# Kernel optimization log

Measured on AMD Instinct MI355X. Metric: run time of the kernel, lower is better.

The kernel has to match this reference:

```python
import jax, jax.numpy as jnp
import numpy as np

N = 11616          # IMDB total nodes (hard-coded slices in source)
NHID = 512
L = 4              # num_layers (encoder and decoder each)
E = 371712         # ~32 avg degree
SIZES = [4278, 2081, 5257]
FEATS = [3066, 2081, 5257]
GAMMA = 3.0


def setup_inputs() -> dict:
    key = jax.random.key(0)
    ks = jax.random.split(key, 24)
    s = 0.02
    d = {}
    d["X0"] = jax.random.normal(ks[0], (SIZES[0], FEATS[0]), jnp.float32)
    d["X1"] = jax.random.normal(ks[1], (SIZES[1], FEATS[1]), jnp.float32)
    d["X2"] = jax.random.normal(ks[2], (SIZES[2], FEATS[2]), jnp.float32)
    d["src"] = jax.random.randint(ks[3], (E,), 0, N)
    d["dst"] = jax.random.randint(ks[4], (E,), 0, N)
    d["edge_w"] = jax.random.uniform(ks[5], (E,), jnp.float32) / 32.0  # ~normalized adjacency values
    d["adj_full"] = (jax.random.uniform(ks[6], (N, N), jnp.float32) < 0.005).astype(jnp.float32)
    # input projections fc_list: feat_dim -> nhid
    for i in range(3):
        d[f"fc_W{i}"] = jax.random.normal(ks[7 + i], (FEATS[i], NHID), jnp.float32) * s
        d[f"fc_b{i}"] = jnp.zeros((NHID,), jnp.float32)
    # stacked GraphConvolution weights (encoder / decoder)
    d["enc_W"] = jax.random.normal(ks[10], (L, NHID, NHID), jnp.float32) * s
    d["enc_b"] = jnp.zeros((L, NHID), jnp.float32)
    d["dec_W"] = jax.random.normal(ks[11], (L, NHID, NHID), jnp.float32) * s
    d["dec_b"] = jnp.zeros((L, NHID), jnp.float32)
    # output projections fc_list2: nhid -> feat_dim
    for i in range(3):
        d[f"out_W{i}"] = jax.random.normal(ks[12 + i], (NHID, FEATS[i]), jnp.float32) * s
        d[f"out_b{i}"] = jnp.zeros((FEATS[i],), jnp.float32)
    return d


def reference(X0, X1, X2, edge_w, adj_full,
              fc_W0, fc_b0, fc_W1, fc_b1, fc_W2, fc_b2,
              enc_W, enc_b, dec_W, dec_b,
              out_W0, out_b0, out_W1, out_b1, out_W2, out_b2,
              src, dst):
    def spmm(h):  # sparse A @ h via edge list
        return jax.ops.segment_sum(h[src] * edge_w[:, None], dst, num_segments=N)

    # per-type input projection, concat over node types -> [N, NHID]
    x = jnp.concatenate([X0 @ fc_W0 + fc_b0,
                         X1 @ fc_W1 + fc_b1,
                         X2 @ fc_W2 + fc_b2], axis=0)

    # encoder then decoder; per source: relu+dropout only at layer 0 (L>1 branch),
    # residual add for layers i>0; dropout is identity in eval mode.
    for W, b in ((enc_W, enc_b), (dec_W, dec_b)):
        for i in range(L):
            h = spmm(x @ W[i]) + b[i]
            x = jax.nn.relu(h) if i == 0 else x + h

    # IMDB slices of final embedding
    e0, e1, e2 = x[:SIZES[0]], x[SIZES[0]:SIZES[0] + SIZES[1]], x[SIZES[0] + SIZES[1]:]
    r0 = e0 @ out_W0 + out_b0
    r1 = e1 @ out_W1 + out_b1
    r2 = e2 @ out_W2 + out_b2

    # emb_loss_fun2: BCE(sigmoid(x x^T), adj_full), mean. Stable form:
    z = x @ x.T  # [N, N]
    emb_loss = jnp.mean(adj_full * jax.nn.softplus(-z) + (1.0 - adj_full) * jax.nn.softplus(z))

    # recon_loss_fun2 on type-0 features (cosine-based, power gamma)
    rn = r0 / jnp.maximum(jnp.linalg.norm(r0, axis=-1, keepdims=True), 1e-12)
    fn = X0 / jnp.maximum(jnp.linalg.norm(X0, axis=1, keepdims=True), 1e-12)
    recon_loss = jnp.mean((1.0 - jnp.sum(rn * fn, axis=-1)) ** GAMMA)

    return (r0, r1, r2, emb_loss, recon_loss)
```

## Files before the change

### kernel.cpp

```cpp
#include <hip/hip_runtime.h>
#include <math.h>

#define N_NODES 11616
#define NROWPAD 11776
#define NHID    512
#define EDGES   371712
#define S0 4278
#define S1 2081
#define S2 5257
#define F0 3066
#define F1 2081
#define F2 5257
#define NBLK 91
#define FC_KS 4

typedef __attribute__((ext_vector_type(8))) short bf16x8;
typedef __attribute__((ext_vector_type(4))) float f32x4;

#define GL2LDS(g, l) __builtin_amdgcn_global_load_lds(                         \
    (const __attribute__((address_space(1))) unsigned int*)(g),                \
    (__attribute__((address_space(3))) unsigned int*)(l), 16, 0, 0)

__device__ __forceinline__ int slot_of(int row, int kg)
{
    return row * 4 + (kg ^ ((row >> 1) & 3));
}

__global__ void k_init(double* __restrict__ accum, int* __restrict__ indeg,
                       int* __restrict__ cursor)
{
    int i = blockIdx.x * blockDim.x + threadIdx.x;
    if (i < 2) accum[i] = 0.0;
    if (i < N_NODES) { indeg[i] = 0; cursor[i] = 0; }
}

__global__ void k_padzero(short* __restrict__ xh, short* __restrict__ xl)
{
    int i = blockIdx.x * blockDim.x + threadIdx.x;
    const int base  = N_NODES * NHID;
    const int total = (NROWPAD - N_NODES) * NHID;
    if (i < total) { xh[base + i] = 0; xl[base + i] = 0; }
}

__global__ void k_count(const int* __restrict__ dst, int* __restrict__ indeg)
{
    int e = blockIdx.x * blockDim.x + threadIdx.x;
    if (e < EDGES) atomicAdd(&indeg[dst[e]], 1);
}

__global__ void k_scan(const int* __restrict__ indeg, int* __restrict__ rowptr)
{
    __shared__ int part[256];
    const int t = threadIdx.x;
    const int chunk = (N_NODES + 255) / 256;
    const int base = t * chunk;
    int s = 0;
    for (int i = 0; i < chunk; ++i) {
        int idx = base + i;
        if (idx < N_NODES) s += indeg[idx];
    }
    part[t] = s;
    __syncthreads();
    if (t == 0) for (int i = 1; i < 256; ++i) part[i] += part[i - 1];
    __syncthreads();
    int run = (t == 0) ? 0 : part[t - 1];
    for (int i = 0; i < chunk; ++i) {
        int idx = base + i;
        if (idx < N_NODES) { rowptr[idx] = run; run += indeg[idx]; }
    }
    if (t == 0) rowptr[N_NODES] = part[255];
}

__global__ void k_fill(const int* __restrict__ src, const int* __restrict__ dst,
                       const float* __restrict__ ew, const int* __restrict__ rowptr,
                       int* __restrict__ cursor, int* __restrict__ csrc,
                       float* __restrict__ cw)
{
    int e = blockIdx.x * blockDim.x + threadIdx.x;
    if (e >= EDGES) return;
    int d = dst[e];
    int pos = rowptr[d] + atomicAdd(&cursor[d], 1);
    csrc[pos] = src[e];
    cw[pos]   = ew[e];
}

__device__ __forceinline__ void split_bf16(float f, short& hi, short& lo)
{
    unsigned u  = __float_as_uint(f);
    unsigned hr = (u + 0x7FFFu + ((u >> 16) & 1u)) & 0xFFFF0000u;
    float    fh = __uint_as_float(hr);
    float    fl = f - fh;
    unsigned ul = __float_as_uint(fl);
    unsigned lr = ul + 0x7FFFu + ((ul >> 16) & 1u);
    hi = (short)(hr >> 16);
    lo = (short)(lr >> 16);
}

__global__ void k_splitpad(const float* __restrict__ in, short* __restrict__ oh,
                           short* __restrict__ ol, int R, int C, int Cpad)
{
    const int c = blockIdx.x * 256 + threadIdx.x;
    const int r = blockIdx.y;
    if (c >= Cpad) return;
    float f = (r < R && c < C) ? in[(long)r * C + c] : 0.f;
    short h, l;
    split_bf16(f, h, l);
    oh[(long)r * Cpad + c] = h;
    ol[(long)r * Cpad + c] = l;
}

__global__ void k_tsplit(const float* __restrict__ in, short* __restrict__ oh,
                         short* __restrict__ ol, int R, int C, int Rpad, int Cpad)
{
    __shared__ float tile[32][33];
    const int cb = blockIdx.x * 32, rb = blockIdx.y * 32;
    const int tx = threadIdx.x, ty = threadIdx.y;
    #pragma unroll
    for (int i = ty; i < 32; i += 8) {
        int r = rb + i, c = cb + tx;
        tile[i][tx] = (r < R && c < C) ? in[(long)r * C + c] : 0.f;
    }
    __syncthreads();
    #pragma unroll
    for (int i = ty; i < 32; i += 8) {
        int row = cb + i, col = rb + tx;
        if (row < Cpad && col < Rpad) {
            short h, l;
            split_bf16(tile[tx][i], h, l);
            oh[(long)row * Rpad + col] = h;
            ol[(long)row * Rpad + col] = l;
        }
    }
}

__device__ __forceinline__ void stage_gl(const short* __restrict__ src, int ldk,
                                         int k0, short* ldsPanel, int lane)
{
    #pragma unroll
    for (int i = 0; i < 8; ++i) {
        int ci  = i * 64 + lane;
        int row = ci >> 2;
        int kgs = (ci & 3) ^ ((row >> 1) & 3);
        const short* g = src + (long)row * ldk + k0 + kgs * 8;
        GL2LDS(g, (char*)ldsPanel + i * 1024);
    }
}

__global__ __launch_bounds__(256, 3)
void k_gemm_bb(const short* __restrict__ Agh, const short* __restrict__ Agl,
               const short* __restrict__ Bgh, const short* __restrict__ Bgl,
               const float* __restrict__ bias, float* __restrict__ C,
               int M, int NN, int Kpad, int ldk)
{
    __shared__ short P[4][4096];
    const int t = threadIdx.x, lane = t & 63, w = t >> 6;
    const int rowBase = blockIdx.y * 128, colBase = blockIdx.x * 128;
    const int wm = (w >> 1) * 64, wn = (w & 1) * 64;
    const int kg = lane >> 4, fr = lane & 15;

    const short* srcs[4] = { Agh + (long)rowBase * ldk, Agl + (long)rowBase * ldk,
                             Bgh + (long)colBase * ldk, Bgl + (long)colBase * ldk };
    const short* mySrc = srcs[w];

    int offA[4], offB[4];
    #pragma unroll
    for (int f = 0; f < 4; ++f) {
        int rA = wm + f * 16 + fr, rB = wn + f * 16 + fr;
        offA[f] = slot_of(rA, kg) * 8;
        offB[f] = slot_of(rB, kg) * 8;
    }

    f32x4 acc[4][4];
    #pragma unroll
    for (int i = 0; i < 4; ++i)
        #pragma unroll
        for (int j = 0; j < 4; ++j)
            acc[i][j] = (f32x4){0.f, 0.f, 0.f, 0.f};

    for (int k0 = 0; k0 < Kpad; k0 += 32) {
        stage_gl(mySrc, ldk, k0, &P[w][0], lane);
        __syncthreads();
        bf16x8 ah[4], al[4], bh[4], bl[4];
        #pragma unroll
        for (int f = 0; f < 4; ++f) {
            ah[f] = *(const bf16x8*)&P[0][offA[f]];
            al[f] = *(const bf16x8*)&P[1][offA[f]];
            bh[f] = *(const bf16x8*)&P[2][offB[f]];
            bl[f] = *(const bf16x8*)&P[3][offB[f]];
        }
        #pragma unroll
        for (int i = 0; i < 4; ++i)
            #pragma unroll
            for (int j = 0; j < 4; ++j) {
                acc[i][j] = __builtin_amdgcn_mfma_f32_16x16x32_bf16(ah[i], bh[j], acc[i][j], 0, 0, 0);
                acc[i][j] = __builtin_amdgcn_mfma_f32_16x16x32_bf16(ah[i], bl[j], acc[i][j], 0, 0, 0);
                acc[i][j] = __builtin_amdgcn_mfma_f32_16x16x32_bf16(al[i], bh[j], acc[i][j], 0, 0, 0);
            }
        __syncthreads();
    }

    #pragma unroll
    for (int i = 0; i < 4; ++i) {
        #pragma unroll
        for (int q = 0; q < 4; ++q) {
            int r = rowBase + wm + i * 16 + kg * 4 + q;
            if (r >= M) continue;
            #pragma unroll
            for (int j = 0; j < 4; ++j) {
                int c = colBase + wn + j * 16 + fr;
                if (c < NN)
                    C[(long)r * NN + c] = acc[i][j][q] + (bias ? bias[c] : 0.f);
            }
        }
    }
}

__global__ __launch_bounds__(256, 3)
void k_gemm_red(const short* __restrict__ Agh, const short* __restrict__ Agl,
                const short* __restrict__ Bgh, const short* __restrict__ Bgl,
                float* __restrict__ Cpart, int M, int ldk, int kChunk)
{
    __shared__ short P[4][4096];
    const int t = threadIdx.x, lane = t & 63, w = t >> 6;
    const int rowBase = blockIdx.y * 128, colBase = blockIdx.x * 128;
    const int z = blockIdx.z;
    const int wm = (w >> 1) * 64, wn = (w & 1) * 64;
    const int kg = lane >> 4, fr = lane & 15;

    const short* srcs[4] = { Agh + (long)rowBase * ldk, Agl + (long)rowBase * ldk,
                             Bgh + (long)colBase * ldk, Bgl + (long)colBase * ldk };
    const short* mySrc = srcs[w];

    int offA[4], offB[4];
    #pragma unroll
    for (int f = 0; f < 4; ++f) {
        int rA = wm + f * 16 + fr, rB = wn + f * 16 + fr;
        offA[f] = slot_of(rA, kg) * 8;
        offB[f] = slot_of(rB, kg) * 8;
    }

    f32x4 acc[4][4];
    #pragma unroll
    for (int i = 0; i < 4; ++i)
        #pragma unroll
        for (int j = 0; j < 4; ++j)
            acc[i][j] = (f32x4){0.f, 0.f, 0.f, 0.f};

    const int kEnd = z * kChunk + kChunk;
    for (int k0 = z * kChunk; k0 < kEnd; k0 += 32) {
        stage_gl(mySrc, ldk, k0, &P[w][0], lane);
        __syncthreads();
        bf16x8 ah[4], al[4], bh[4], bl[4];
        #pragma unroll
        for (int f = 0; f < 4; ++f) {
            ah[f] = *(const bf16x8*)&P[0][offA[f]];
            al[f] = *(const bf16x8*)&P[1][offA[f]];
            bh[f] = *(const bf16x8*)&P[2][offB[f]];
            bl[f] = *(const bf16x8*)&P[3][offB[f]];
        }
        #pragma unroll
        for (int i = 0; i < 4; ++i)
            #pragma unroll
            for (int j = 0; j < 4; ++j) {
                acc[i][j] = __builtin_amdgcn_mfma_f32_16x16x32_bf16(ah[i], bh[j], acc[i][j], 0, 0, 0);
                acc[i][j] = __builtin_amdgcn_mfma_f32_16x16x32_bf16(ah[i], bl[j], acc[i][j], 0, 0, 0);
                acc[i][j] = __builtin_amdgcn_mfma_f32_16x16x32_bf16(al[i], bh[j], acc[i][j], 0, 0, 0);
            }
        __syncthreads();
    }

    #pragma unroll
    for (int i = 0; i < 4; ++i) {
        #pragma unroll
        for (int q = 0; q < 4; ++q) {
            int r = rowBase + wm + i * 16 + kg * 4 + q;
            if (r >= M) continue;
            #pragma unroll
            for (int j = 0; j < 4; ++j) {
                int c = colBase + wn + j * 16 + fr;
                Cpart[((long)z * M + r) * NHID + c] = acc[i][j][q];
            }
        }
    }
}

__global__ void k_fcreduce(const float* __restrict__ Cpart, const float* __restrict__ bias,
                           int M, float* __restrict__ xo, short* __restrict__ oh,
                           short* __restrict__ ol)
{
    const int r = blockIdx.x;
    const int c = threadIdx.x << 2;
    float4 s = *reinterpret_cast<const float4*>(bias + c);
    #pragma unroll
    for (int z = 0; z < FC_KS; ++z) {
        const float4 p = *reinterpret_cast<const float4*>(Cpart + ((long)z * M + r) * NHID + c);
        s.x += p.x; s.y += p.y; s.z += p.z; s.w += p.w;
    }
    *reinterpret_cast<float4*>(xo + (long)r * NHID + c) = s;
    short4 h, l;
    split_bf16(s.x, h.x, l.x); split_bf16(s.y, h.y, l.y);
    split_bf16(s.z, h.z, l.z); split_bf16(s.w, h.w, l.w);
    *reinterpret_cast<short4*>(oh + (long)r * NHID + c) = h;
    *reinterpret_cast<short4*>(ol + (long)r * NHID + c) = l;
}

__global__ __launch_bounds__(256, 3)
void k_zloss(const short* __restrict__ xh, const short* __restrict__ xl,
             const float* __restrict__ adj, double* __restrict__ accum)
{
    __shared__ short P[4][4096];
    __shared__ float ztr[4][16][17];
    __shared__ float red[256];
    const int t = threadIdx.x, lane = t & 63, w = t >> 6;

    int b = blockIdx.x, R = 0;
    while (b >= NBLK - R) { b -= NBLK - R; ++R; }
    const int Cb = R + b;
    const int rowBase = R * 128, colBase = Cb * 128;
    const int diag = (Cb == R);

    const int wm = (w >> 1) * 64, wn = (w & 1) * 64;
    const int kg = lane >> 4, fr = lane & 15;

    const short* srcs[4] = { xh + (long)rowBase * NHID, xl + (long)rowBase * NHID,
                             xh + (long)colBase * NHID, xl + (long)colBase * NHID };
    const short* mySrc = srcs[w];

    int offA[4], offB[4];
    #pragma unroll
    for (int f = 0; f < 4; ++f) {
        int rA = wm + f * 16 + fr, rB = wn + f * 16 + fr;
        offA[f] = slot_of(rA, kg) * 8;
        offB[f] = slot_of(rB, kg) * 8;
    }

    f32x4 acc[4][4];
    #pragma unroll
    for (int i = 0; i < 4; ++i)
        #pragma unroll
        for (int j = 0; j < 4; ++j)
            acc[i][j] = (f32x4){0.f, 0.f, 0.f, 0.f};

    for (int k0 = 0; k0 < NHID; k0 += 32) {
        stage_gl(mySrc, NHID, k0, &P[w][0], lane);
        __syncthreads();
        bf16x8 ah[4], al[4], bh[4], bl[4];
        #pragma unroll
        for (int f = 0; f < 4; ++f) {
            ah[f] = *(const bf16x8*)&P[0][offA[f]];
            al[f] = *(const bf16x8*)&P[1][offA[f]];
            bh[f] = *(const bf16x8*)&P[2][offB[f]];
            bl[f] = *(const bf16x8*)&P[3][offB[f]];
        }
        #pragma unroll
        for (int i = 0; i < 4; ++i)
            #pragma unroll
            for (int j = 0; j < 4; ++j) {
                acc[i][j] = __builtin_amdgcn_mfma_f32_16x16x32_bf16(ah[i], bh[j], acc[i][j], 0, 0, 0);
                acc[i][j] = __builtin_amdgcn_mfma_f32_16x16x32_bf16(ah[i], bl[j], acc[i][j], 0, 0, 0);
                acc[i][j] = __builtin_amdgcn_mfma_f32_16x16x32_bf16(al[i], bh[j], acc[i][j], 0, 0, 0);
            }
        __syncthreads();
    }

    float local = 0.f;
    #pragma unroll
    for (int i = 0; i < 4; ++i) {
        #pragma unroll
        for (int q = 0; q < 4; ++q) {
            int r = rowBase + wm + i * 16 + kg * 4 + q;
            if (r >= N_NODES) continue;
            #pragma unroll
            for (int j = 0; j < 4; ++j) {
                int c = colBase + wn + j * 16 + fr;
                if (c >= N_NODES) continue;
                float z  = acc[i][j][q];
                float e  = __expf(-fabsf(z));
                float sp = fmaxf(z, 0.f) + __logf(1.f + e);
                float a1 = adj[(long)r * N_NODES + c];
                local += diag ? (sp - a1 * z) : (2.f * sp - a1 * z);
            }
        }
    }
    if (!diag) {
        #pragma unroll
        for (int i = 0; i < 4; ++i) {
            #pragma unroll
            for (int j = 0; j < 4; ++j) {
                #pragma unroll
                for (int q = 0; q < 4; ++q)
                    ztr[w][kg * 4 + q][fr] = acc[i][j][q];
                #pragma unroll
                for (int q = 0; q < 4; ++q) {
                    float zt = ztr[w][fr][kg * 4 + q];
                    int cc = colBase + wn + j * 16 + kg * 4 + q;
                    int rr = rowBase + wm + i * 16 + fr;
                    if (cc < N_NODES && rr < N_NODES)
                        local -= adj[(long)cc * N_NODES + rr] * zt;
                }
            }
        }
    }
    red[t] = local;
    __syncthreads();
    for (int sft = 128; sft > 0; sft >>= 1) {
        if (t < sft) red[t] += red[t + sft];
        __syncthreads();
    }
    if (t == 0) atomicAdd(accum, (double)red[0]);
}

__global__ void k_spmm(const float* __restrict__ y, const float* __restrict__ xold,
                       const int* __restrict__ rowptr, const int* __restrict__ csrc,
                       const float* __restrict__ cw, const float* __restrict__ bias,
                       int do_relu, float* __restrict__ xnew,
                       short* __restrict__ xh, short* __restrict__ xl)
{
    const int wv   = threadIdx.x >> 6;
    const int lane = threadIdx.x & 63;
    const int n    = blockIdx.x * 4 + wv;
    const int c1   = lane << 2;
    const int c2   = c1 + 256;
    float4 s1 = make_float4(0.f, 0.f, 0.f, 0.f);
    float4 s2 = make_float4(0.f, 0.f, 0.f, 0.f);
    const int beg = rowptr[n], end = rowptr[n + 1];
    for (int e = beg; e < end; ++e) {
        int   sn = csrc[e];
        float wt = cw[e];
        const float* yr = y + (long)sn * NHID;
        const float4 y1 = *reinterpret_cast<const float4*>(yr + c1);
        const float4 y2 = *reinterpret_cast<const float4*>(yr + c2);
        s1.x = fmaf(wt, y1.x, s1.x); s1.y = fmaf(wt, y1.y, s1.y);
        s1.z = fmaf(wt, y1.z, s1.z); s1.w = fmaf(wt, y1.w, s1.w);
        s2.x = fmaf(wt, y2.x, s2.x); s2.y = fmaf(wt, y2.y, s2.y);
        s2.z = fmaf(wt, y2.z, s2.z); s2.w = fmaf(wt, y2.w, s2.w);
    }
    const float4 b1 = *reinterpret_cast<const float4*>(bias + c1);
    const float4 b2 = *reinterpret_cast<const float4*>(bias + c2);
    float4 o1, o2;
    o1.x = s1.x + b1.x; o1.y = s1.y + b1.y; o1.z = s1.z + b1.z; o1.w = s1.w + b1.w;
    o2.x = s2.x + b2.x; o2.y = s2.y + b2.y; o2.z = s2.z + b2.z; o2.w = s2.w + b2.w;
    if (do_relu) {
        o1.x = fmaxf(o1.x, 0.f); o1.y = fmaxf(o1.y, 0.f);
        o1.z = fmaxf(o1.z, 0.f); o1.w = fmaxf(o1.w, 0.f);
        o2.x = fmaxf(o2.x, 0.f); o2.y = fmaxf(o2.y, 0.f);
        o2.z = fmaxf(o2.z, 0.f); o2.w = fmaxf(o2.w, 0.f);
    } else {
        const float4 x1 = *reinterpret_cast<const float4*>(xold + (long)n * NHID + c1);
        const float4 x2 = *reinterpret_cast<const float4*>(xold + (long)n * NHID + c2);
        o1.x += x1.x; o1.y += x1.y; o1.z += x1.z; o1.w += x1.w;
        o2.x += x2.x; o2.y += x2.y; o2.z += x2.z; o2.w += x2.w;
    }
    *reinterpret_cast<float4*>(xnew + (long)n * NHID + c1) = o1;
    *reinterpret_cast<float4*>(xnew + (long)n * NHID + c2) = o2;
    short4 h, l;
    split_bf16(o1.x, h.x, l.x); split_bf16(o1.y, h.y, l.y);
    split_bf16(o1.z, h.z, l.z); split_bf16(o1.w, h.w, l.w);
    *reinterpret_cast<short4*>(xh + (long)n * NHID + c1) = h;
    *reinterpret_cast<short4*>(xl + (long)n * NHID + c1) = l;
    split_bf16(o2.x, h.x, l.x); split_bf16(o2.y, h.y, l.y);
    split_bf16(o2.z, h.z, l.z); split_bf16(o2.w, h.w, l.w);
    *reinterpret_cast<short4*>(xh + (long)n * NHID + c2) = h;
    *reinterpret_cast<short4*>(xl + (long)n * NHID + c2) = l;
}

__global__ void k_recon(const float* __restrict__ r0, const float* __restrict__ X0,
                        double* __restrict__ accum)
{
    const int row = blockIdx.x;
    const int t = threadIdx.x;
    float dot = 0.f, nr = 0.f, nf = 0.f;
    for (int c = t; c < F0; c += 256) {
        float a = r0[(long)row * F0 + c];
        float b = X0[(long)row * F0 + c];
        dot = fmaf(a, b, dot);
        nr  = fmaf(a, a, nr);
        nf  = fmaf(b, b, nf);
    }
    #pragma unroll
    for (int o = 32; o > 0; o >>= 1) {
        dot += __shfl_down(dot, o);
        nr  += __shfl_down(nr, o);
        nf  += __shfl_down(nf, o);
    }
    __shared__ float sd[3][4];
    const int lane = t & 63, wid = t >> 6;
    if (lane == 0) { sd[0][wid] = dot; sd[1][wid] = nr; sd[2][wid] = nf; }
    __syncthreads();
    if (t == 0) {
        float d = sd[0][0] + sd[0][1] + sd[0][2] + sd[0][3];
        float a = sd[1][0] + sd[1][1] + sd[1][2] + sd[1][3];
        float b = sd[2][0] + sd[2][1] + sd[2][2] + sd[2][3];
        float cosv = d / (fmaxf(sqrtf(a), 1e-12f) * fmaxf(sqrtf(b), 1e-12f));
        float v = 1.f - cosv;
        atomicAdd(accum + 1, (double)(v * v * v));
    }
}

__global__ void k_final(const double* __restrict__ accum, float* __restrict__ out)
{
    if (threadIdx.x == 0) {
        out[45082958] = (float)(accum[0] / ((double)N_NODES * (double)N_NODES));
        out[45082959] = (float)(accum[1] / (double)S0);
    }
}

extern "C" void kernel_launch(void* const* d_in, const int* in_sizes, int n_in,
                              void* d_out, int out_size, void* d_ws, size_t ws_size,
                              hipStream_t stream)
{
    const float* X0  = (const float*)d_in[0];
    const float* X1  = (const float*)d_in[1];
    const float* X2  = (const float*)d_in[2];
    const int*   src = (const int*)d_in[3];
    const int*   dst = (const int*)d_in[4];
    const float* ew  = (const float*)d_in[5];
    const float* adj = (const float*)d_in[6];
    const float* fcW[3]  = {(const float*)d_in[7],  (const float*)d_in[9],  (const float*)d_in[11]};
    const float* fcB[3]  = {(const float*)d_in[8],  (const float*)d_in[10], (const float*)d_in[12]};
    const float* encW = (const float*)d_in[13];
    const float* encB = (const float*)d_in[14];
    const float* decW = (const float*)d_in[15];
    const float* decB = (const float*)d_in[16];
    const float* outW[3] = {(const float*)d_in[17], (const float*)d_in[19], (const float*)d_in[21]};
    const float* outB[3] = {(const float*)d_in[18], (const float*)d_in[20], (const float*)d_in[22]};
    float* out = (float*)d_out;

    const int FD[3]     = {F0, F1, F2};
    const int FPAD[3]   = {(F0 + 127) & ~127, (F1 + 127) & ~127, (F2 + 127) & ~127};
    const int SPAD[3]   = {(S0 + 127) & ~127, (S1 + 127) & ~127, (S2 + 127) & ~127};
    const int SD[3]     = {S0, S1, S2};
    const float* XD[3]  = {X0, X1, X2};

    char* ws = (char*)d_ws;
    size_t off = 0;
    auto alloc = [&](size_t bytes) { void* p = ws + off; off += (bytes + 255) & ~(size_t)255; return p; };

    double* accum = (double*)alloc(16);
    const size_t XB = (size_t)N_NODES * NHID * sizeof(float);
    float* xbuf = (float*)alloc(XB);
    float* ybuf = (float*)alloc(XB);
    float* xalt = (float*)alloc(XB);
    short* xh   = (short*)alloc((size_t)NROWPAD * NHID * 2);
    short* xl   = (short*)alloc((size_t)NROWPAD * NHID * 2);
    const size_t XSmax = (size_t)5376 * 5376;
    short* Xsh  = (short*)alloc(XSmax * 2);
    short* Xsl  = (short*)alloc(XSmax * 2);
    short* fcWh = (short*)alloc((size_t)NHID * 5376 * 2);
    short* fcWl = (short*)alloc((size_t)NHID * 5376 * 2);
    short* wTh  = (short*)alloc((size_t)8 * NHID * NHID * 2);
    short* wTl  = (short*)alloc((size_t)8 * NHID * NHID * 2);
    int* indeg  = (int*)alloc((size_t)N_NODES * 4);
    int* rowptr = (int*)alloc((size_t)(N_NODES + 1) * 4);
    int* cursor = (int*)alloc((size_t)N_NODES * 4);
    int* csrc   = (int*)alloc((size_t)EDGES * 4);
    float* cw   = (float*)alloc((size_t)EDGES * 4);

    float* cpart = ybuf;

    k_init<<<dim3((N_NODES + 255) / 256), dim3(256), 0, stream>>>(accum, indeg, cursor);
    k_padzero<<<dim3(((NROWPAD - N_NODES) * NHID + 255) / 256), dim3(256), 0, stream>>>(xh, xl);
    k_count<<<dim3((EDGES + 255) / 256), dim3(256), 0, stream>>>(dst, indeg);
    k_scan<<<dim3(1), dim3(256), 0, stream>>>(indeg, rowptr);
    k_fill<<<dim3((EDGES + 255) / 256), dim3(256), 0, stream>>>(src, dst, ew, rowptr, cursor, csrc, cw);

    auto tgrid = [](int Cpad, int Rpad) { return dim3((unsigned)((Cpad + 31) / 32), (unsigned)((Rpad + 31) / 32)); };
    auto ggrid = [](int m, int nn) { return dim3((unsigned)((nn + 127) / 128), (unsigned)((m + 127) / 128)); };

    for (int i = 0; i < 4; ++i) {
        k_tsplit<<<tgrid(NHID, NHID), dim3(32, 8), 0, stream>>>(
            encW + (size_t)i * NHID * NHID, wTh + (size_t)i * NHID * NHID,
            wTl + (size_t)i * NHID * NHID, NHID, NHID, NHID, NHID);
        k_tsplit<<<tgrid(NHID, NHID), dim3(32, 8), 0, stream>>>(
            decW + (size_t)i * NHID * NHID, wTh + (size_t)(4 + i) * NHID * NHID,
            wTl + (size_t)(4 + i) * NHID * NHID, NHID, NHID, NHID, NHID);
    }

    {
        size_t rowoff = 0;
        for (int i = 0; i < 3; ++i) {
            k_splitpad<<<dim3((FPAD[i] + 255) / 256, SPAD[i]), dim3(256), 0, stream>>>(
                XD[i], Xsh, Xsl, SD[i], FD[i], FPAD[i]);
            k_tsplit<<<tgrid(NHID, FPAD[i]), dim3(32, 8), 0, stream>>>(
                fcW[i], fcWh, fcWl, FD[i], NHID, FPAD[i], NHID);
            k_gemm_red<<<dim3(NHID / 128, SPAD[i] / 128, FC_KS), dim3(256), 0, stream>>>(
                Xsh, Xsl, fcWh, fcWl, cpart, SD[i], FPAD[i], FPAD[i] / FC_KS);
            k_fcreduce<<<dim3(SD[i]), dim3(128), 0, stream>>>(
                cpart, fcB[i], SD[i], xbuf + rowoff * NHID,
                xh + rowoff * NHID, xl + rowoff * NHID);
            rowoff += SD[i];
        }
    }

    float* x  = xbuf;
    float* xn = xalt;
    for (int phase = 0; phase < 2; ++phase) {
        const float* B = phase ? decB : encB;
        for (int i = 0; i < 4; ++i) {
            k_gemm_bb<<<ggrid(N_NODES, NHID), dim3(256), 0, stream>>>(
                xh, xl, wTh + (size_t)(phase * 4 + i) * NHID * NHID,
                wTl + (size_t)(phase * 4 + i) * NHID * NHID,
                nullptr, ybuf, N_NODES, NHID, NHID, NHID);
            k_spmm<<<dim3(N_NODES / 4), dim3(256), 0, stream>>>(
                ybuf, x, rowptr, csrc, cw, B + (size_t)i * NHID, (i == 0) ? 1 : 0,
                xn, xh, xl);
            float* tmp = x; x = xn; xn = tmp;
        }
    }

    short* oWh = Xsh;
    short* oWl = Xsl;
    {
        short *ph = oWh, *pl = oWl;
        for (int i = 0; i < 3; ++i) {
            int FDP = (FD[i] + 127) & ~127;
            k_tsplit<<<tgrid(FDP, NHID), dim3(32, 8), 0, stream>>>(
                outW[i], ph, pl, NHID, FD[i], NHID, FDP);
            ph += (size_t)FDP * NHID; pl += (size_t)FDP * NHID;
        }
    }

    {
        short *ph = oWh, *pl = oWl;
        float* oo = out;
        size_t rowoff = 0;
        for (int i = 0; i < 3; ++i) {
            int FDP = (FD[i] + 127) & ~127;
            k_gemm_bb<<<ggrid(SD[i], FD[i]), dim3(256), 0, stream>>>(
                xh + rowoff * NHID, xl + rowoff * NHID, ph, pl, outB[i], oo,
                SD[i], FD[i], NHID, NHID);
            ph += (size_t)FDP * NHID; pl += (size_t)FDP * NHID;
            oo += (size_t)SD[i] * FD[i];
            rowoff += SD[i];
        }
    }

    k_zloss<<<dim3(NBLK * (NBLK + 1) / 2), dim3(256), 0, stream>>>(xh, xl, adj, accum);
    k_recon<<<dim3(S0), dim3(256), 0, stream>>>(out, X0, accum);
    k_final<<<dim3(1), dim3(64), 0, stream>>>(accum, out);
}
```

Before: 2.300 ms.

## Alias zloss shared memory, raise occupancy, and split SpMM across column slices

The z-loss kernel now places its staging buffer and its epilogue scratch (transpose tile and reduction array) in one shared-memory union, and its launch bound moves from 3 to 4 blocks per SM. The epilogue is restructured so that the forward and transposed adjacency terms are handled in the same i/j loop. The SpMM kernel is split into 8 column slices of 64 floats, each lane handling one scalar column, which gives eight times more blocks and fewer registers per thread. The cost is that edge indices and weights are re-read by every slice, and SpMM memory accesses become scalar instead of float4.

```diff
diff --git a/kernel.cpp b/kernel.cpp
--- a/kernel.cpp
+++ b/kernel.cpp
@@ -304,13 +304,14 @@
     *reinterpret_cast<short4*>(ol + (long)r * NHID + c) = l;
 }
 
-__global__ __launch_bounds__(256, 3)
+__global__ __launch_bounds__(256, 4)
 void k_zloss(const short* __restrict__ xh, const short* __restrict__ xl,
              const float* __restrict__ adj, double* __restrict__ accum)
 {
-    __shared__ short P[4][4096];
-    __shared__ float ztr[4][16][17];
-    __shared__ float red[256];
+    __shared__ union {
+        short P[4][4096];
+        struct { float ztr[4][16][17]; float red[256]; } e;
+    } U;
     const int t = threadIdx.x, lane = t & 63, w = t >> 6;
 
     int b = blockIdx.x, R = 0;
@@ -342,15 +343,15 @@
             acc[i][j] = (f32x4){0.f, 0.f, 0.f, 0.f};
 
     for (int k0 = 0; k0 < NHID; k0 += 32) {
-        stage_gl(mySrc, NHID, k0, &P[w][0], lane);
+        stage_gl(mySrc, NHID, k0, &U.P[w][0], lane);
         __syncthreads();
         bf16x8 ah[4], al[4], bh[4], bl[4];
         #pragma unroll
         for (int f = 0; f < 4; ++f) {
-            ah[f] = *(const bf16x8*)&P[0][offA[f]];
-            al[f] = *(const bf16x8*)&P[1][offA[f]];
-            bh[f] = *(const bf16x8*)&P[2][offB[f]];
-            bl[f] = *(const bf16x8*)&P[3][offB[f]];
+            ah[f] = *(const bf16x8*)&U.P[0][offA[f]];
+            al[f] = *(const bf16x8*)&U.P[1][offA[f]];
+            bh[f] = *(const bf16x8*)&U.P[2][offB[f]];
+            bl[f] = *(const bf16x8*)&U.P[3][offB[f]];
         }
         #pragma unroll
         for (int i = 0; i < 4; ++i)
@@ -367,47 +368,44 @@
     #pragma unroll
     for (int i = 0; i < 4; ++i) {
         #pragma unroll
-        for (int q = 0; q < 4; ++q) {
-            int r = rowBase + wm + i * 16 + kg * 4 + q;
-            if (r >= N_NODES) continue;
-            #pragma unroll
-            for (int j = 0; j < 4; ++j) {
-                int c = colBase + wn + j * 16 + fr;
-                if (c >= N_NODES) continue;
-                float z  = acc[i][j][q];
-                float e  = __expf(-fabsf(z));
-                float sp = fmaxf(z, 0.f) + __logf(1.f + e);
-                float a1 = adj[(long)r * N_NODES + c];
-                local += diag ? (sp - a1 * z) : (2.f * sp - a1 * z);
-            }
-        }
-    }
-    if (!diag) {
-        #pragma unroll
-        for (int i = 0; i < 4; ++i) {
-            #pragma unroll
-            for (int j = 0; j < 4; ++j) {
+        for (int j = 0; j < 4; ++j) {
+            const int rbase = rowBase + wm + i * 16;
+            const int cbase = colBase + wn + j * 16;
+            if (!diag) {
                 #pragma unroll
                 for (int q = 0; q < 4; ++q)
-                    ztr[w][kg * 4 + q][fr] = acc[i][j][q];
+                    U.e.ztr[w][kg * 4 + q][fr] = acc[i][j][q];
+            }
+            #pragma unroll
+            for (int q = 0; q < 4; ++q) {
+                float z  = acc[i][j][q];
+                float sp = fmaxf(z, 0.f) + __logf(1.f + __expf(-fabsf(z)));
+                int r = rbase + kg * 4 + q, c = cbase + fr;
+                if (r < N_NODES && c < N_NODES) {
+                    float a1 = adj[(long)r * N_NODES + c];
+                    local += diag ? (sp - a1 * z) : (2.f * sp - a1 * z);
+                }
+            }
+            if (!diag) {
                 #pragma unroll
                 for (int q = 0; q < 4; ++q) {
-                    float zt = ztr[w][fr][kg * 4 + q];
-                    int cc = colBase + wn + j * 16 + kg * 4 + q;
-                    int rr = rowBase + wm + i * 16 + fr;
+                    float zt = U.e.ztr[w][fr][kg * 4 + q];
+                    int cc = cbase + kg * 4 + q;
+                    int rr = rbase + fr;
                     if (cc < N_NODES && rr < N_NODES)
                         local -= adj[(long)cc * N_NODES + rr] * zt;
                 }
             }
         }
     }
-    red[t] = local;
+    __syncthreads();
+    U.e.red[t] = local;
     __syncthreads();
     for (int sft = 128; sft > 0; sft >>= 1) {
-        if (t < sft) red[t] += red[t + sft];
+        if (t < sft) U.e.red[t] += U.e.red[t + sft];
         __syncthreads();
     }
-    if (t == 0) atomicAdd(accum, (double)red[0]);
+    if (t == 0) atomicAdd(accum, (double)U.e.red[0]);
 }
 
 __global__ void k_spmm(const float* __restrict__ y, const float* __restrict__ xold,
@@ -416,52 +414,27 @@
                        int do_relu, float* __restrict__ xnew,
                        short* __restrict__ xh, short* __restrict__ xl)
 {
-    const int wv   = threadIdx.x >> 6;
-    const int lane = threadIdx.x & 63;
-    const int n    = blockIdx.x * 4 + wv;
-    const int c1   = lane << 2;
-    const int c2   = c1 + 256;
-    float4 s1 = make_float4(0.f, 0.f, 0.f, 0.f);
-    float4 s2 = make_float4(0.f, 0.f, 0.f, 0.f);
+    const int slice = blockIdx.x / (N_NODES / 4);
+    const int ng    = blockIdx.x % (N_NODES / 4);
+    const int wv    = threadIdx.x >> 6;
+    const int lane  = threadIdx.x & 63;
+    const int n     = ng * 4 + wv;
+    const int c     = slice * 64 + lane;
+    float s = 0.f;
     const int beg = rowptr[n], end = rowptr[n + 1];
     for (int e = beg; e < end; ++e) {
         int   sn = csrc[e];
         float wt = cw[e];
-        const float* yr = y + (long)sn * NHID;
-        const float4 y1 = *reinterpret_cast<const float4*>(yr + c1);
-        const float4 y2 = *reinterpret_cast<const float4*>(yr + c2);
-        s1.x = fmaf(wt, y1.x, s1.x); s1.y = fmaf(wt, y1.y, s1.y);
-        s1.z = fmaf(wt, y1.z, s1.z); s1.w = fmaf(wt, y1.w, s1.w);
-        s2.x = fmaf(wt, y2.x, s2.x); s2.y = fmaf(wt, y2.y, s2.y);
-        s2.z = fmaf(wt, y2.z, s2.z); s2.w = fmaf(wt, y2.w, s2.w);
-    }
-    const float4 b1 = *reinterpret_cast<const float4*>(bias + c1);
-    const float4 b2 = *reinterpret_cast<const float4*>(bias + c2);
-    float4 o1, o2;
-    o1.x = s1.x + b1.x; o1.y = s1.y + b1.y; o1.z = s1.z + b1.z; o1.w = s1.w + b1.w;
-    o2.x = s2.x + b2.x; o2.y = s2.y + b2.y; o2.z = s2.z + b2.z; o2.w = s2.w + b2.w;
-    if (do_relu) {
-        o1.x = fmaxf(o1.x, 0.f); o1.y = fmaxf(o1.y, 0.f);
-        o1.z = fmaxf(o1.z, 0.f); o1.w = fmaxf(o1.w, 0.f);
-        o2.x = fmaxf(o2.x, 0.f); o2.y = fmaxf(o2.y, 0.f);
-        o2.z = fmaxf(o2.z, 0.f); o2.w = fmaxf(o2.w, 0.f);
-    } else {
-        const float4 x1 = *reinterpret_cast<const float4*>(xold + (long)n * NHID + c1);
-        const float4 x2 = *reinterpret_cast<const float4*>(xold + (long)n * NHID + c2);
-        o1.x += x1.x; o1.y += x1.y; o1.z += x1.z; o1.w += x1.w;
-        o2.x += x2.x; o2.y += x2.y; o2.z += x2.z; o2.w += x2.w;
-    }
-    *reinterpret_cast<float4*>(xnew + (long)n * NHID + c1) = o1;
-    *reinterpret_cast<float4*>(xnew + (long)n * NHID + c2) = o2;
-    short4 h, l;
-    split_bf16(o1.x, h.x, l.x); split_bf16(o1.y, h.y, l.y);
-    split_bf16(o1.z, h.z, l.z); split_bf16(o1.w, h.w, l.w);
-    *reinterpret_cast<short4*>(xh + (long)n * NHID + c1) = h;
-    *reinterpret_cast<short4*>(xl + (long)n * NHID + c1) = l;
-    split_bf16(o2.x, h.x, l.x); split_bf16(o2.y, h.y, l.y);
-    split_bf16(o2.z, h.z, l.z); split_bf16(o2.w, h.w, l.w);
-    *reinterpret_cast<short4*>(xh + (long)n * NHID + c2) = h;
-    *reinterpret_cast<short4*>(xl + (long)n * NHID + c2) = l;
+        s = fmaf(wt, y[(long)sn * NHID + c], s);
+    }
+    float o = s + bias[c];
+    if (do_relu) o = fmaxf(o, 0.f);
+    else         o += xold[(long)n * NHID + c];
+    xnew[(long)n * NHID + c] = o;
+    short h, l;
+    split_bf16(o, h, l);
+    xh[(long)n * NHID + c] = h;
+    xl[(long)n * NHID + c] = l;
 }
 
 __global__ void k_recon(const float* __restrict__ r0, const float* __restrict__ X0,
@@ -601,7 +574,7 @@
                 xh, xl, wTh + (size_t)(phase * 4 + i) * NHID * NHID,
                 wTl + (size_t)(phase * 4 + i) * NHID * NHID,
                 nullptr, ybuf, N_NODES, NHID, NHID, NHID);
-            k_spmm<<<dim3(N_NODES / 4), dim3(256), 0, stream>>>(
+            k_spmm<<<dim3((N_NODES / 4) * 8), dim3(256), 0, stream>>>(
                 ybuf, x, rowptr, csrc, cw, B + (size_t)i * NHID, (i == 0) ? 1 : 0,
                 xn, xh, xl);
             float* tmp = x; x = xn; xn = tmp;
```

Result: slower. 3.380 ms (+47.0%).
